# Optimization experiments

Hardware: AMD Instinct MI355X
Metric: run time of the kernel (lower is better)

## Reference

```python
import jax, jax.numpy as jnp
import numpy as np

DIM = 1024
NUM_HEADS = 16
HEAD_DIM = DIM // NUM_HEADS
SCALE = HEAD_DIM ** -0.5


def setup_inputs() -> dict:
    key = jax.random.key(0)
    ks = jax.random.split(key, 5)
    B, N, C = 2, 2048, DIM
    x = jax.random.normal(ks[0], (B, N, C), dtype=jnp.float32)
    s = 1.0 / np.sqrt(C)
    W_qkv = jax.random.normal(ks[1], (C, 3 * C), dtype=jnp.float32) * s
    b_qkv = jax.random.normal(ks[2], (3 * C,), dtype=jnp.float32) * 0.01
    W_proj = jax.random.normal(ks[3], (C, C), dtype=jnp.float32) * s
    b_proj = jax.random.normal(ks[4], (C,), dtype=jnp.float32) * 0.01
    return {"x": x, "W_qkv": W_qkv, "b_qkv": b_qkv, "W_proj": W_proj, "b_proj": b_proj}


def reference(x, W_qkv, b_qkv, W_proj, b_proj):
    B, N, C = x.shape
    qkv = x @ W_qkv + b_qkv                      # [B, N, 3C]
    qkv = qkv.reshape(B, N, 3, NUM_HEADS, HEAD_DIM)
    qkv = jnp.transpose(qkv, (2, 0, 3, 1, 4))    # [3, B, H, N, hd]
    # Faithful to source quirk: q = k = v = qkv[2]
    v = qkv[2]
    q = v
    k = v
    attn = jnp.einsum('bhnd,bhmd->bhnm', q, k) * SCALE
    attn = jax.nn.softmax(attn, axis=-1)
    out = jnp.einsum('bhnm,bhmd->bhnd', attn, v)  # [B, H, N, hd]
    out = jnp.transpose(out, (0, 2, 1, 3)).reshape(B, N, C)
    return out @ W_proj + b_proj
```

## Files before the change

### kernel.cpp

```cpp
#include <hip/hip_runtime.h>

typedef __bf16    bf16x4 __attribute__((ext_vector_type(4)));
typedef __bf16    bf16x8 __attribute__((ext_vector_type(8)));
typedef _Float16  f16x2  __attribute__((ext_vector_type(2)));
typedef _Float16  f16x4  __attribute__((ext_vector_type(4)));
typedef _Float16  f16x8  __attribute__((ext_vector_type(8)));
typedef float     f32x4  __attribute__((ext_vector_type(4)));

#define MFMA16x16x32 __builtin_amdgcn_mfma_f32_16x16x32_bf16
#define MFMA16x16x16F __builtin_amdgcn_mfma_f32_16x16x16f16

__device__ __forceinline__ void gload_lds16(const void* g, void* l) {
  __builtin_amdgcn_global_load_lds((const __attribute__((address_space(1))) void*)g,
                                   (__attribute__((address_space(3))) void*)l, 16, 0, 0);
}

__device__ __forceinline__ f16x2 pkrtz(float a, float b) {
  return __builtin_bit_cast(f16x2, __builtin_amdgcn_cvt_pkrtz(a, b));
}

__global__ __launch_bounds__(256) void prep_transpose(const float* __restrict__ Wqkv,
                                                      const float* __restrict__ Wproj,
                                                      __bf16* __restrict__ WvT,
                                                      __bf16* __restrict__ WpT) {
  __shared__ float tile[64][65];
  const float* src; __bf16* dst; int ld, c0;
  if (blockIdx.z == 0) { src = Wqkv; dst = WvT; ld = 3072; c0 = 2048; }
  else                 { src = Wproj; dst = WpT; ld = 1024; c0 = 0; }
  const int k0 = blockIdx.x * 64, n0 = blockIdx.y * 64;
  const int t = threadIdx.x;
#pragma unroll
  for (int i = 0; i < 4; i++) {
    int idx = t + i * 256; int r = idx >> 4, g = idx & 15;
    float4 v = *(const float4*)&src[(size_t)(k0 + r) * ld + c0 + n0 + g * 4];
    tile[r][g * 4 + 0] = v.x; tile[r][g * 4 + 1] = v.y;
    tile[r][g * 4 + 2] = v.z; tile[r][g * 4 + 3] = v.w;
  }
  __syncthreads();
#pragma unroll
  for (int i = 0; i < 4; i++) {
    int idx = t + i * 256; int n = idx >> 4, g = idx & 15;
    bf16x4 o;
    o.x = (__bf16)tile[g * 4 + 0][n]; o.y = (__bf16)tile[g * 4 + 1][n];
    o.z = (__bf16)tile[g * 4 + 2][n]; o.w = (__bf16)tile[g * 4 + 3][n];
    *(bf16x4*)&dst[(size_t)(n0 + n) * 1024 + k0 + g * 4] = o;
  }
}

__global__ __launch_bounds__(256, 4) void gemm_v(const float* __restrict__ x,
                                                 const __bf16* __restrict__ WvT,
                                                 const float* __restrict__ bias,
                                                 __bf16* __restrict__ V,
                                                 _Float16* __restrict__ Vt) {
  constexpr int K = 1024;
  __shared__ char lds[2 * 12288];
  const int t = threadIdx.x, w = t >> 6, l = t & 63, lr = l & 15, quad = l >> 4;
  const int m0 = blockIdx.x * 64, n0 = blockIdx.y * 64;

  const int rmA = t >> 3;
  const int kgAs = (t & 7) ^ (rmA & 7);
  const float* pA0 = x + (size_t)(m0 + rmA) * K + kgAs * 4;
  const float* pA1 = pA0 + (size_t)32 * K;
  const int rnB = t >> 2, kgB = t & 3;
  const __bf16* pB = WvT + (size_t)(n0 + rnB) * K + kgB * 8;

  f32x4 acc[4] = {};
  {
    char* buf = (char*)lds;
    gload_lds16(pA0, buf + t * 16);
    gload_lds16(pA1, buf + (t + 256) * 16);
    gload_lds16(pB, buf + 8192 + t * 16);
  }
  const int rr = w * 16 + lr;
  const int ga0 = rr * 8 + ((2 * quad) ^ (rr & 7));
  const int ga1 = rr * 8 + ((2 * quad + 1) ^ (rr & 7));
  for (int it = 0; it < 32; ++it) {
    __syncthreads();
    if (it + 1 < 32) {
      pA0 += 32; pA1 += 32; pB += 32;
      char* buf = (char*)lds + ((it + 1) & 1) * 12288;
      gload_lds16(pA0, buf + t * 16);
      gload_lds16(pA1, buf + (t + 256) * 16);
      gload_lds16(pB, buf + 8192 + t * 16);
    }
    const char* Abuf = (char*)lds + (it & 1) * 12288;
    const char* Bbuf = Abuf + 8192;
    f32x4 a0 = *(const f32x4*)(Abuf + ga0 * 16);
    f32x4 a1 = *(const f32x4*)(Abuf + ga1 * 16);
    bf16x8 af;
    af[0] = (__bf16)a0[0]; af[1] = (__bf16)a0[1]; af[2] = (__bf16)a0[2]; af[3] = (__bf16)a0[3];
    af[4] = (__bf16)a1[0]; af[5] = (__bf16)a1[1]; af[6] = (__bf16)a1[2]; af[7] = (__bf16)a1[3];
#pragma unroll
    for (int nc = 0; nc < 4; nc++) {
      bf16x8 bv = *(const bf16x8*)(Bbuf + (nc * 16 + lr) * 64 + quad * 16);
      acc[nc] = MFMA16x16x32(af, bv, acc[nc], 0, 0, 0);
    }
  }
  const int b_ = blockIdx.x >> 5, by = blockIdx.y;
  const int ntok0 = (m0 & 2047) + w * 16 + quad * 4;
#pragma unroll
  for (int nc = 0; nc < 4; nc++) {
    int gcol = n0 + nc * 16 + lr;
    float bb = bias[gcol];
    float v0 = acc[nc][0] + bb, v1 = acc[nc][1] + bb;
    float v2 = acc[nc][2] + bb, v3 = acc[nc][3] + bb;
#pragma unroll
    for (int r = 0; r < 4; r++) {
      int grow = m0 + w * 16 + quad * 4 + r;
      float vv = (r == 0) ? v0 : (r == 1) ? v1 : (r == 2) ? v2 : v3;
      V[(size_t)grow * 1024 + gcol] = (__bf16)vv;
    }
    f16x2 lo = pkrtz(v0, v1), hi = pkrtz(v2, v3);
    f16x4 pv; pv[0] = lo[0]; pv[1] = lo[1]; pv[2] = hi[0]; pv[3] = hi[1];
    *(f16x4*)&Vt[((size_t)(b_ * 16 + by) * 64 + nc * 16 + lr) * 2048 + ntok0] = pv;
  }
}

__global__ __launch_bounds__(256, 4) void gemm_proj(const __bf16* __restrict__ A,
                                                    const __bf16* __restrict__ Bt,
                                                    const float* __restrict__ bias,
                                                    float* __restrict__ outp) {
  constexpr int K = 1024, Nn = 1024;
  __shared__ __bf16 lds[2 * 4096];
  const int t = threadIdx.x, w = t >> 6, l = t & 63, lr = l & 15, quad = l >> 4;
  const int m0 = blockIdx.x * 64, n0 = blockIdx.y * 64;
  const int rm = t >> 2, kg = t & 3;

  const __bf16* pA = A  + (size_t)(m0 + rm) * K + kg * 8;
  const __bf16* pB = Bt + (size_t)(n0 + rm) * K + kg * 8;

  f32x4 acc[4] = {};
  gload_lds16(pA, (char*)lds + t * 16);
  gload_lds16(pB, (char*)lds + 4096 + t * 16);
  for (int it = 0; it < 32; ++it) {
    __syncthreads();
    if (it + 1 < 32) {
      pA += 32; pB += 32;
      char* buf = (char*)lds + ((it + 1) & 1) * 8192;
      gload_lds16(pA, buf + t * 16);
      gload_lds16(pB, buf + 4096 + t * 16);
    }
    const __bf16* Al = lds + (it & 1) * 4096;
    const __bf16* Bl = Al + 2048;
    bf16x8 af = *(const bf16x8*)&Al[(w * 16 + lr) * 32 + quad * 8];
#pragma unroll
    for (int nc = 0; nc < 4; nc++) {
      bf16x8 bv = *(const bf16x8*)&Bl[(nc * 16 + lr) * 32 + quad * 8];
      acc[nc] = MFMA16x16x32(af, bv, acc[nc], 0, 0, 0);
    }
  }
#pragma unroll
  for (int nc = 0; nc < 4; nc++)
#pragma unroll
    for (int r = 0; r < 4; r++) {
      int grow = m0 + w * 16 + quad * 4 + r;
      int gcol = n0 + nc * 16 + lr;
      outp[(size_t)grow * Nn + gcol] = acc[nc][r] + bias[gcol];
    }
}

__global__ __launch_bounds__(512, 4) void attn_kernel(const __bf16* __restrict__ V,
                                                      const _Float16* __restrict__ Vt,
                                                      __bf16* __restrict__ O) {
  __shared__ char lds[65536];
  const int t = threadIdx.x, w = t >> 6, l = t & 63, lr = l & 15, quad = l >> 4;
  const int bh = blockIdx.x, b = bh >> 4, h = bh & 15;
  const int qb = blockIdx.y * 128 + (w & 3) * 16;
  const int part = w >> 2;

  const __bf16* Vbh = V + (size_t)b * 2048 * 1024 + h * 64;
  const _Float16* Vtbh = Vt + (size_t)bh * 64 * 2048;

  bf16x8 qf[2][2];
#pragma unroll
  for (int sub = 0; sub < 2; sub++)
#pragma unroll
    for (int ks = 0; ks < 2; ks++)
      qf[sub][ks] = *(const bf16x8*)(Vbh + (size_t)(qb + sub * 64 + lr) * 1024 + ks * 32 + quad * 8);

  const int kva = t >> 3, ua = (t & 7) ^ (kva & 7);
  const __bf16* pK0 = Vbh + (size_t)kva * 1024 + ua * 8;
  const __bf16* pK1 = pK0 + (size_t)64 * 1024;
  const int kb_ = t >> 7, d_ = (t >> 1) & 63, qh = (t & 1) ^ ((d_ >> 2) & 1);
  const _Float16* pV0 = Vtbh + (size_t)d_ * 2048 + kb_ * 16 + qh * 8;
  const _Float16* pV1 = pV0 + 64;

  const int koff0 = lr * 128 + ((quad ^ (lr & 7)) * 16);
  const int koff1 = lr * 128 + (((4 + quad) ^ (lr & 7)) * 16);
  const int xq = (quad >> 1) ^ ((lr >> 2) & 1);
  const int voff = lr * 32 + xq * 16 + (quad & 1) * 8;

  f32x4 o[2][4] = {};
  f32x4 l5[2] = {};
  f16x4 ones; ones[0] = ones[1] = ones[2] = ones[3] = (_Float16)1.0f;
  const float Cc = 0.18033688011112042f;
  const float C8 = 11.541560327111707f;

  {
    char* base = lds;
    gload_lds16(pK0, base + t * 16);
    gload_lds16(pV0, base + 8192 + t * 16);
    gload_lds16(pK1, base + 16384 + t * 16);
    gload_lds16(pV1, base + 24576 + t * 16);
  }
  for (int it = 0; it < 16; ++it) {
    __syncthreads();
    if (it + 1 < 16) {
      pK0 += 131072; pK1 += 131072; pV0 += 128; pV1 += 128;
      char* base = lds + ((it + 1) & 1) * 32768;
      gload_lds16(pK0, base + t * 16);
      gload_lds16(pV0, base + 8192 + t * 16);
      gload_lds16(pK1, base + 16384 + t * 16);
      gload_lds16(pV1, base + 24576 + t * 16);
    }
    const char* Kb = lds + (it & 1) * 32768 + part * 16384;
    const char* Vb = Kb + 8192;

    f32x4 s[2][4] = {};
    __builtin_amdgcn_s_setprio(1);
#pragma unroll
    for (int ks = 0; ks < 2; ks++) {
      const int ko = ks ? koff1 : koff0;
#pragma unroll
      for (int rb = 0; rb < 4; rb++) {
        bf16x8 kf = *(const bf16x8*)(Kb + ko + rb * 2048);
        s[0][rb] = MFMA16x16x32(kf, qf[0][ks], s[0][rb], 0, 0, 0);
        s[1][rb] = MFMA16x16x32(kf, qf[1][ks], s[1][rb], 0, 0, 0);
      }
    }
    __builtin_amdgcn_s_setprio(0);

    f16x4 pf[2][4];
#pragma unroll
    for (int sub = 0; sub < 2; sub++)
#pragma unroll
      for (int rb = 0; rb < 4; rb++) {
        float p0 = __builtin_amdgcn_exp2f(s[sub][rb][0] * Cc - C8);
        float p1 = __builtin_amdgcn_exp2f(s[sub][rb][1] * Cc - C8);
        float p2 = __builtin_amdgcn_exp2f(s[sub][rb][2] * Cc - C8);
        float p3 = __builtin_amdgcn_exp2f(s[sub][rb][3] * Cc - C8);
        f16x2 lo = pkrtz(p0, p1);
        f16x2 hi = pkrtz(p2, p3);
        pf[sub][rb][0] = lo[0]; pf[sub][rb][1] = lo[1];
        pf[sub][rb][2] = hi[0]; pf[sub][rb][3] = hi[1];
      }

    __builtin_amdgcn_s_setprio(1);
#pragma unroll
    for (int kb = 0; kb < 4; kb++) {
#pragma unroll
      for (int db = 0; db < 4; db++) {
        f16x4 vf = *(const f16x4*)(Vb + voff + db * 512 + kb * 2048);
        o[0][db] = MFMA16x16x16F(pf[0][kb], vf, o[0][db], 0, 0, 0);
        o[1][db] = MFMA16x16x16F(pf[1][kb], vf, o[1][db], 0, 0, 0);
      }
      l5[0] = MFMA16x16x16F(pf[0][kb], ones, l5[0], 0, 0, 0);
      l5[1] = MFMA16x16x16F(pf[1][kb], ones, l5[1], 0, 0, 0);
    }
    __builtin_amdgcn_s_setprio(0);
  }

  __syncthreads();
  float* xch = (float*)lds;
  if (w >= 4) {
    float* dsto = xch + (w - 4) * 2048;
#pragma unroll
    for (int sub = 0; sub < 2; sub++)
#pragma unroll
      for (int db = 0; db < 4; db++)
        *(f32x4*)&dsto[(sub * 4 + db) * 256 + l * 4] = o[sub][db];
    float* dstl = xch + 8192 + (w - 4) * 512;
    *(f32x4*)&dstl[l * 4] = l5[0];
    *(f32x4*)&dstl[256 + l * 4] = l5[1];
  }
  __syncthreads();
  if (w < 4) {
    const float* srco = xch + w * 2048;
    const float* srcl = xch + 8192 + w * 512;
#pragma unroll
    for (int sub = 0; sub < 2; sub++) {
#pragma unroll
      for (int db = 0; db < 4; db++)
        o[sub][db] += *(const f32x4*)&srco[(sub * 4 + db) * 256 + l * 4];
      l5[sub] += *(const f32x4*)&srcl[sub * 256 + l * 4];
    }
#pragma unroll
    for (int sub = 0; sub < 2; sub++)
#pragma unroll
      for (int r = 0; r < 4; r++) {
        float lv = 1.0f / l5[sub][r];
        int token = b * 2048 + qb + sub * 64 + quad * 4 + r;
#pragma unroll
        for (int db = 0; db < 4; db++)
          O[(size_t)token * 1024 + h * 64 + db * 16 + lr] = (__bf16)(o[sub][db][r] * lv);
      }
  }
}

extern "C" void kernel_launch(void* const* d_in, const int* in_sizes, int n_in,
                              void* d_out, int out_size, void* d_ws, size_t ws_size,
                              hipStream_t stream) {
  (void)in_sizes; (void)n_in; (void)out_size; (void)ws_size;
  const float* x     = (const float*)d_in[0];
  const float* Wqkv  = (const float*)d_in[1];
  const float* bqkv  = (const float*)d_in[2];
  const float* Wproj = (const float*)d_in[3];
  const float* bproj = (const float*)d_in[4];

  char* ws = (char*)d_ws;
  __bf16*    V   = (__bf16*)(ws);
  _Float16*  Vt  = (_Float16*)(ws + (size_t)8  * 1048576);
  __bf16*    Ob  = (__bf16*)(ws + (size_t)16 * 1048576);
  __bf16*    WvT = (__bf16*)(ws + (size_t)24 * 1048576);
  __bf16*    WpT = (__bf16*)(ws + (size_t)26 * 1048576);

  prep_transpose<<<dim3(16, 16, 2), 256, 0, stream>>>(Wqkv, Wproj, WvT, WpT);
  gemm_v<<<dim3(64, 16), 256, 0, stream>>>(x, WvT, bqkv + 2048, V, Vt);
  attn_kernel<<<dim3(32, 16), 512, 0, stream>>>(V, Vt, Ob);
  gemm_proj<<<dim3(64, 16), 256, 0, stream>>>(Ob, WpT, bproj, (float*)d_out);
}
```

Baseline: 169.0 us.

## Pre-cast x to bf16 and enlarge GEMM tiles to 128x64 with 2x2 waves

Adds a separate kernel that casts x to bf16 once, so gemm_v loads bf16 A tiles instead of converting fp32 in its inner loop. Both GEMMs now use 128x64 block tiles with a 2x2 wave layout, each wave holding 4x2 accumulators, which raises operand reuse per LDS read and halves the grid. The s_setprio hints in the attention loop are removed. The costs are an extra launch plus a full pass over x through memory, fewer blocks (512) for occupancy, and xb sharing a workspace slot with Ob, which is safe only because Ob is written after gemm_v has read xb.

```diff
diff --git a/kernel.cpp b/kernel.cpp
--- a/kernel.cpp
+++ b/kernel.cpp
@@ -17,6 +17,15 @@
 
 __device__ __forceinline__ f16x2 pkrtz(float a, float b) {
   return __builtin_bit_cast(f16x2, __builtin_amdgcn_cvt_pkrtz(a, b));
+}
+
+__global__ __launch_bounds__(256) void xcast(const float* __restrict__ x,
+                                             __bf16* __restrict__ xb) {
+  const int gid = blockIdx.x * 256 + threadIdx.x;
+  float4 v = ((const float4*)x)[gid];
+  bf16x4 o;
+  o.x = (__bf16)v.x; o.y = (__bf16)v.y; o.z = (__bf16)v.z; o.w = (__bf16)v.w;
+  *(bf16x4*)&xb[(size_t)gid * 4] = o;
 }
 
 __global__ __launch_bounds__(256) void prep_transpose(const float* __restrict__ Wqkv,
@@ -47,7 +56,7 @@
   }
 }
 
-__global__ __launch_bounds__(256, 4) void gemm_v(const float* __restrict__ x,
+__global__ __launch_bounds__(256, 2) void gemm_v(const __bf16* __restrict__ xb,
                                                  const __bf16* __restrict__ WvT,
                                                  const float* __restrict__ bias,
                                                  __bf16* __restrict__ V,
@@ -55,108 +64,126 @@
   constexpr int K = 1024;
   __shared__ char lds[2 * 12288];
   const int t = threadIdx.x, w = t >> 6, l = t & 63, lr = l & 15, quad = l >> 4;
-  const int m0 = blockIdx.x * 64, n0 = blockIdx.y * 64;
-
-  const int rmA = t >> 3;
-  const int kgAs = (t & 7) ^ (rmA & 7);
-  const float* pA0 = x + (size_t)(m0 + rmA) * K + kgAs * 4;
-  const float* pA1 = pA0 + (size_t)32 * K;
-  const int rnB = t >> 2, kgB = t & 3;
-  const __bf16* pB = WvT + (size_t)(n0 + rnB) * K + kgB * 8;
-
-  f32x4 acc[4] = {};
+  const int wr = w >> 1, wc = w & 1;
+  const int m0 = blockIdx.x * 128, n0 = blockIdx.y * 64;
+
+  const int rA = t >> 2, kg = t & 3;
+  const __bf16* pA0 = xb + (size_t)(m0 + rA) * K + kg * 8;
+  const __bf16* pA1 = pA0 + (size_t)64 * K;
+  const __bf16* pB  = WvT + (size_t)(n0 + rA) * K + kg * 8;
+
+  f32x4 acc[4][2] = {};
   {
     char* buf = (char*)lds;
     gload_lds16(pA0, buf + t * 16);
-    gload_lds16(pA1, buf + (t + 256) * 16);
-    gload_lds16(pB, buf + 8192 + t * 16);
-  }
-  const int rr = w * 16 + lr;
-  const int ga0 = rr * 8 + ((2 * quad) ^ (rr & 7));
-  const int ga1 = rr * 8 + ((2 * quad + 1) ^ (rr & 7));
+    gload_lds16(pA1, buf + 4096 + t * 16);
+    gload_lds16(pB,  buf + 8192 + t * 16);
+  }
   for (int it = 0; it < 32; ++it) {
     __syncthreads();
     if (it + 1 < 32) {
       pA0 += 32; pA1 += 32; pB += 32;
       char* buf = (char*)lds + ((it + 1) & 1) * 12288;
       gload_lds16(pA0, buf + t * 16);
-      gload_lds16(pA1, buf + (t + 256) * 16);
-      gload_lds16(pB, buf + 8192 + t * 16);
-    }
-    const char* Abuf = (char*)lds + (it & 1) * 12288;
+      gload_lds16(pA1, buf + 4096 + t * 16);
+      gload_lds16(pB,  buf + 8192 + t * 16);
+    }
+    const char* Abuf = (const char*)lds + (it & 1) * 12288;
     const char* Bbuf = Abuf + 8192;
-    f32x4 a0 = *(const f32x4*)(Abuf + ga0 * 16);
-    f32x4 a1 = *(const f32x4*)(Abuf + ga1 * 16);
-    bf16x8 af;
-    af[0] = (__bf16)a0[0]; af[1] = (__bf16)a0[1]; af[2] = (__bf16)a0[2]; af[3] = (__bf16)a0[3];
-    af[4] = (__bf16)a1[0]; af[5] = (__bf16)a1[1]; af[6] = (__bf16)a1[2]; af[7] = (__bf16)a1[3];
-#pragma unroll
-    for (int nc = 0; nc < 4; nc++) {
-      bf16x8 bv = *(const bf16x8*)(Bbuf + (nc * 16 + lr) * 64 + quad * 16);
-      acc[nc] = MFMA16x16x32(af, bv, acc[nc], 0, 0, 0);
-    }
-  }
-  const int b_ = blockIdx.x >> 5, by = blockIdx.y;
-  const int ntok0 = (m0 & 2047) + w * 16 + quad * 4;
-#pragma unroll
-  for (int nc = 0; nc < 4; nc++) {
-    int gcol = n0 + nc * 16 + lr;
-    float bb = bias[gcol];
-    float v0 = acc[nc][0] + bb, v1 = acc[nc][1] + bb;
-    float v2 = acc[nc][2] + bb, v3 = acc[nc][3] + bb;
-#pragma unroll
-    for (int r = 0; r < 4; r++) {
-      int grow = m0 + w * 16 + quad * 4 + r;
-      float vv = (r == 0) ? v0 : (r == 1) ? v1 : (r == 2) ? v2 : v3;
-      V[(size_t)grow * 1024 + gcol] = (__bf16)vv;
-    }
-    f16x2 lo = pkrtz(v0, v1), hi = pkrtz(v2, v3);
-    f16x4 pv; pv[0] = lo[0]; pv[1] = lo[1]; pv[2] = hi[0]; pv[3] = hi[1];
-    *(f16x4*)&Vt[((size_t)(b_ * 16 + by) * 64 + nc * 16 + lr) * 2048 + ntok0] = pv;
-  }
-}
-
-__global__ __launch_bounds__(256, 4) void gemm_proj(const __bf16* __restrict__ A,
+    bf16x8 af[4], bv[2];
+#pragma unroll
+    for (int mi = 0; mi < 4; mi++)
+      af[mi] = *(const bf16x8*)(Abuf + (wr * 64 + mi * 16 + lr) * 64 + quad * 16);
+#pragma unroll
+    for (int nc = 0; nc < 2; nc++)
+      bv[nc] = *(const bf16x8*)(Bbuf + (wc * 32 + nc * 16 + lr) * 64 + quad * 16);
+#pragma unroll
+    for (int mi = 0; mi < 4; mi++)
+#pragma unroll
+      for (int nc = 0; nc < 2; nc++)
+        acc[mi][nc] = MFMA16x16x32(af[mi], bv[nc], acc[mi][nc], 0, 0, 0);
+  }
+  const int by = blockIdx.y;
+#pragma unroll
+  for (int mi = 0; mi < 4; mi++) {
+    const int grow0 = m0 + wr * 64 + mi * 16 + quad * 4;
+    const int b_ = grow0 >> 11, tok0 = grow0 & 2047;
+#pragma unroll
+    for (int nc = 0; nc < 2; nc++) {
+      const int d = wc * 32 + nc * 16 + lr;
+      const int gcol = n0 + d;
+      float bb = bias[gcol];
+      float v0 = acc[mi][nc][0] + bb, v1 = acc[mi][nc][1] + bb;
+      float v2 = acc[mi][nc][2] + bb, v3 = acc[mi][nc][3] + bb;
+      V[(size_t)(grow0 + 0) * 1024 + gcol] = (__bf16)v0;
+      V[(size_t)(grow0 + 1) * 1024 + gcol] = (__bf16)v1;
+      V[(size_t)(grow0 + 2) * 1024 + gcol] = (__bf16)v2;
+      V[(size_t)(grow0 + 3) * 1024 + gcol] = (__bf16)v3;
+      f16x2 lo = pkrtz(v0, v1), hi = pkrtz(v2, v3);
+      f16x4 pv; pv[0] = lo[0]; pv[1] = lo[1]; pv[2] = hi[0]; pv[3] = hi[1];
+      *(f16x4*)&Vt[((size_t)(b_ * 16 + by) * 64 + d) * 2048 + tok0] = pv;
+    }
+  }
+}
+
+__global__ __launch_bounds__(256, 2) void gemm_proj(const __bf16* __restrict__ A,
                                                     const __bf16* __restrict__ Bt,
                                                     const float* __restrict__ bias,
                                                     float* __restrict__ outp) {
   constexpr int K = 1024, Nn = 1024;
-  __shared__ __bf16 lds[2 * 4096];
+  __shared__ char lds[2 * 12288];
   const int t = threadIdx.x, w = t >> 6, l = t & 63, lr = l & 15, quad = l >> 4;
-  const int m0 = blockIdx.x * 64, n0 = blockIdx.y * 64;
-  const int rm = t >> 2, kg = t & 3;
-
-  const __bf16* pA = A  + (size_t)(m0 + rm) * K + kg * 8;
-  const __bf16* pB = Bt + (size_t)(n0 + rm) * K + kg * 8;
-
-  f32x4 acc[4] = {};
-  gload_lds16(pA, (char*)lds + t * 16);
-  gload_lds16(pB, (char*)lds + 4096 + t * 16);
+  const int wr = w >> 1, wc = w & 1;
+  const int m0 = blockIdx.x * 128, n0 = blockIdx.y * 64;
+
+  const int rA = t >> 2, kg = t & 3;
+  const __bf16* pA0 = A + (size_t)(m0 + rA) * K + kg * 8;
+  const __bf16* pA1 = pA0 + (size_t)64 * K;
+  const __bf16* pB  = Bt + (size_t)(n0 + rA) * K + kg * 8;
+
+  f32x4 acc[4][2] = {};
+  {
+    char* buf = (char*)lds;
+    gload_lds16(pA0, buf + t * 16);
+    gload_lds16(pA1, buf + 4096 + t * 16);
+    gload_lds16(pB,  buf + 8192 + t * 16);
+  }
   for (int it = 0; it < 32; ++it) {
     __syncthreads();
     if (it + 1 < 32) {
-      pA += 32; pB += 32;
-      char* buf = (char*)lds + ((it + 1) & 1) * 8192;
-      gload_lds16(pA, buf + t * 16);
-      gload_lds16(pB, buf + 4096 + t * 16);
-    }
-    const __bf16* Al = lds + (it & 1) * 4096;
-    const __bf16* Bl = Al + 2048;
-    bf16x8 af = *(const bf16x8*)&Al[(w * 16 + lr) * 32 + quad * 8];
-#pragma unroll
-    for (int nc = 0; nc < 4; nc++) {
-      bf16x8 bv = *(const bf16x8*)&Bl[(nc * 16 + lr) * 32 + quad * 8];
-      acc[nc] = MFMA16x16x32(af, bv, acc[nc], 0, 0, 0);
-    }
-  }
-#pragma unroll
-  for (int nc = 0; nc < 4; nc++)
-#pragma unroll
-    for (int r = 0; r < 4; r++) {
-      int grow = m0 + w * 16 + quad * 4 + r;
-      int gcol = n0 + nc * 16 + lr;
-      outp[(size_t)grow * Nn + gcol] = acc[nc][r] + bias[gcol];
-    }
+      pA0 += 32; pA1 += 32; pB += 32;
+      char* buf = (char*)lds + ((it + 1) & 1) * 12288;
+      gload_lds16(pA0, buf + t * 16);
+      gload_lds16(pA1, buf + 4096 + t * 16);
+      gload_lds16(pB,  buf + 8192 + t * 16);
+    }
+    const char* Abuf = (const char*)lds + (it & 1) * 12288;
+    const char* Bbuf = Abuf + 8192;
+    bf16x8 af[4], bv[2];
+#pragma unroll
+    for (int mi = 0; mi < 4; mi++)
+      af[mi] = *(const bf16x8*)(Abuf + (wr * 64 + mi * 16 + lr) * 64 + quad * 16);
+#pragma unroll
+    for (int nc = 0; nc < 2; nc++)
+      bv[nc] = *(const bf16x8*)(Bbuf + (wc * 32 + nc * 16 + lr) * 64 + quad * 16);
+#pragma unroll
+    for (int mi = 0; mi < 4; mi++)
+#pragma unroll
+      for (int nc = 0; nc < 2; nc++)
+        acc[mi][nc] = MFMA16x16x32(af[mi], bv[nc], acc[mi][nc], 0, 0, 0);
+  }
+#pragma unroll
+  for (int mi = 0; mi < 4; mi++) {
+    const int grow0 = m0 + wr * 64 + mi * 16 + quad * 4;
+#pragma unroll
+    for (int nc = 0; nc < 2; nc++) {
+      const int gcol = n0 + wc * 32 + nc * 16 + lr;
+      float bb = bias[gcol];
+#pragma unroll
+      for (int r = 0; r < 4; r++)
+        outp[(size_t)(grow0 + r) * Nn + gcol] = acc[mi][nc][r] + bb;
+    }
+  }
 }
 
 __global__ __launch_bounds__(512, 4) void attn_kernel(const __bf16* __restrict__ V,
@@ -217,7 +244,6 @@
     const char* Vb = Kb + 8192;
 
     f32x4 s[2][4] = {};
-    __builtin_amdgcn_s_setprio(1);
 #pragma unroll
     for (int ks = 0; ks < 2; ks++) {
       const int ko = ks ? koff1 : koff0;
@@ -228,7 +254,6 @@
         s[1][rb] = MFMA16x16x32(kf, qf[1][ks], s[1][rb], 0, 0, 0);
       }
     }
-    __builtin_amdgcn_s_setprio(0);
 
     f16x4 pf[2][4];
 #pragma unroll
@@ -245,7 +270,6 @@
         pf[sub][rb][2] = hi[0]; pf[sub][rb][3] = hi[1];
       }
 
-    __builtin_amdgcn_s_setprio(1);
 #pragma unroll
     for (int kb = 0; kb < 4; kb++) {
 #pragma unroll
@@ -257,7 +281,6 @@
       l5[0] = MFMA16x16x16F(pf[0][kb], ones, l5[0], 0, 0, 0);
       l5[1] = MFMA16x16x16F(pf[1][kb], ones, l5[1], 0, 0, 0);
     }
-    __builtin_amdgcn_s_setprio(0);
   }
 
   __syncthreads();
@@ -311,11 +334,13 @@
   __bf16*    V   = (__bf16*)(ws);
   _Float16*  Vt  = (_Float16*)(ws + (size_t)8  * 1048576);
   __bf16*    Ob  = (__bf16*)(ws + (size_t)16 * 1048576);
+  __bf16*    xb  = (__bf16*)(ws + (size_t)16 * 1048576);
   __bf16*    WvT = (__bf16*)(ws + (size_t)24 * 1048576);
   __bf16*    WpT = (__bf16*)(ws + (size_t)26 * 1048576);
 
+  xcast<<<dim3(4096), 256, 0, stream>>>(x, xb);
   prep_transpose<<<dim3(16, 16, 2), 256, 0, stream>>>(Wqkv, Wproj, WvT, WpT);
-  gemm_v<<<dim3(64, 16), 256, 0, stream>>>(x, WvT, bqkv + 2048, V, Vt);
+  gemm_v<<<dim3(32, 16), 256, 0, stream>>>(xb, WvT, bqkv + 2048, V, Vt);
   attn_kernel<<<dim3(32, 16), 512, 0, stream>>>(V, Vt, Ob);
-  gemm_proj<<<dim3(64, 16), 256, 0, stream>>>(Ob, WpT, bproj, (float*)d_out);
-}
+  gemm_proj<<<dim3(32, 16), 256, 0, stream>>>(Ob, WpT, bproj, (float*)d_out);
+}
```

Measured after the change: 162.5 us. -3.8%, faster.
